# Optimization experiments

Hardware: AMD Instinct MI355X
Metric: run time of the kernel (lower is better)

## Reference

```python
import jax, jax.numpy as jnp
import numpy as np

ROUTING_ITERATIONS = 3
EPS = 1e-8


def squash(s):
    # standard CapsNet squash along the last (channels_per_unit) axis
    sq = jnp.sum(s * s, axis=-1, keepdims=True)
    return (sq / (1.0 + sq)) * s / jnp.sqrt(sq + EPS)


def setup_inputs() -> dict:
    key = jax.random.key(0)
    k1, k2 = jax.random.split(key)
    # inputs: (batch, input_channels, input_units)
    inputs = jax.random.normal(k1, (32, 8, 1152), dtype=jnp.float32)
    # weights: (input_units, num_units, input_channels, channels_per_unit)
    weights = jax.random.normal(k2, (1152, 10, 8, 16), dtype=jnp.float32)
    return {"inputs": inputs, "weights": weights}


def reference(inputs, weights):
    # (B, C, U) -> (B, U, C)
    votes = jnp.transpose(inputs, (0, 2, 1))
    # broadcast to (B, U, N, C, D): elementwise product as in the torch code
    pondered = weights[None, :, :, :, :] * votes[:, :, None, :, None]
    logits = jnp.zeros_like(pondered)
    out = pondered  # placeholder; overwritten in first iteration
    for _ in range(ROUTING_ITERATIONS):
        couplings = jax.nn.softmax(logits, axis=-1)
        out = squash(couplings * pondered)
        logits = logits + pondered * out  # agreement update
    # (B, U, N, C, D) -> (B, N, U, C, D)
    return jnp.transpose(out, (0, 2, 1, 3, 4))
```

## Files before the change

kernel.cpp:

```cpp
#include <hip/hip_runtime.h>

#define BB 32
#define UU 1152
#define NN 10
#define CC 8
#define DD 16
#define EPS 1e-8f
#define INV_LN2 1.44269504088896341f


typedef float f32x4 __attribute__((ext_vector_type(4)));

__device__ __forceinline__ float rcp_fast(float x) { return __builtin_amdgcn_rcpf(x); }
__device__ __forceinline__ float rsq_fast(float x) { return __builtin_amdgcn_rsqf(x); }

#if __has_builtin(__builtin_amdgcn_exp2f)
__device__ __forceinline__ float exp2_fast(float x) { return __builtin_amdgcn_exp2f(x); }
#else
__device__ __forceinline__ float exp2_fast(float x) { return __expf(x * 0.6931471805599453f); }
#endif

__device__ __forceinline__ float pair_sum(float x) {
    float y = __int_as_float(
        __builtin_amdgcn_update_dpp(0, __float_as_int(x), 0xB1, 0xF, 0xF, true));
    return x + y;
}

__device__ __forceinline__ float hsum4(f32x4 a) {
    return (a.x + a.y) + (a.z + a.w);
}

__device__ __forceinline__ f32x4 exp2_v4(f32x4 a) {
    f32x4 r;
    r.x = exp2_fast(a.x); r.y = exp2_fast(a.y);
    r.z = exp2_fast(a.z); r.w = exp2_fast(a.w);
    return r;
}

__global__ __launch_bounds__(256) void caps_route_kernel(
    const float* __restrict__ inputs,
    const float* __restrict__ weights,
    float* __restrict__ out)
{
    int tid = threadIdx.x;
    int bi  = blockIdx.x;
    int b   = bi & 31;
    int ub  = bi >> 5;

    int sub    = tid & 1;
    int c      = (tid >> 1) & 7;
    int ulocal = tid >> 4;
    int u      = ub * 16 + ulocal;

    float v = inputs[(b * CC + c) * UU + u];

    const float* wbase = weights + (u * NN * CC + c) * DD + sub * 8;
    float*       obase = out + ((b * NN * UU + u) * CC + c) * DD + sub * 8;
    const int WSTRIDE = CC * DD;
    const int OSTRIDE = UU * CC * DD;

    f32x4 wa0 = *reinterpret_cast<const f32x4*>(wbase);
    f32x4 wb0 = *reinterpret_cast<const f32x4*>(wbase + 4);
    f32x4 wa1 = *reinterpret_cast<const f32x4*>(wbase + WSTRIDE);
    f32x4 wb1 = *reinterpret_cast<const f32x4*>(wbase + WSTRIDE + 4);

    #pragma unroll 1
    for (int n = 0; n < NN; ++n) {
        f32x4 wa = wa0, wb = wb0;
        wa0 = wa1; wb0 = wb1;
        int np = (n + 2 < NN) ? (n + 2) : (NN - 1);
        wa1 = *reinterpret_cast<const f32x4*>(wbase + np * WSTRIDE);
        wb1 = *reinterpret_cast<const f32x4*>(wbase + np * WSTRIDE + 4);

        f32x4 pa = wa * v, pb = wb * v;
        f32x4 qa = pa * pa, qb = pb * pb;

        float sq0 = pair_sum(hsum4(qa + qb)) * (1.0f / 256.0f);
        float kk = sq0 * rcp_fast(1.0f + sq0) * rsq_fast(sq0 + EPS)
                   * (INV_LN2 / 16.0f);
        f32x4 La = kk * qa, Lb = kk * qb;

        {
            f32x4 ea = exp2_v4(La), eb = exp2_v4(Lb);
            float S = pair_sum(hsum4(ea + eb));
            f32x4 ma = ea * qa, mb = eb * qb;
            float A = pair_sum(hsum4(ma * ea + mb * eb));
            float Ssq = S * S;
            float k = A * rsq_fast(fmaf(EPS, Ssq, A)) * rcp_fast(Ssq + A)
                      * INV_LN2;
            La += k * ma;  Lb += k * mb;
        }

        {
            f32x4 ea = exp2_v4(La), eb = exp2_v4(Lb);
            float S = pair_sum(hsum4(ea + eb));
            f32x4 ta = ea * pa, tb = eb * pb;
            float A = pair_sum(hsum4(ta * ta + tb * tb));
            float Ssq = S * S;
            float ko = A * rsq_fast(fmaf(EPS, Ssq, A)) * rcp_fast(Ssq + A);
            *reinterpret_cast<f32x4*>(obase + n * OSTRIDE)     = ko * ta;
            *reinterpret_cast<f32x4*>(obase + n * OSTRIDE + 4) = ko * tb;
        }
    }
}

extern "C" void kernel_launch(void* const* d_in, const int* in_sizes, int n_in,
                              void* d_out, int out_size, void* d_ws, size_t ws_size,
                              hipStream_t stream) {
    const float* inputs  = (const float*)d_in[0];
    const float* weights = (const float*)d_in[1];
    float* out = (float*)d_out;

    const long long total = (long long)BB * UU * CC * 2;
    const int block = 256;
    const int grid = (int)(total / block);
    caps_route_kernel<<<grid, block, 0, stream>>>(inputs, weights, out);
}
```

Before: 43.52 us.

## Precompute per-slice weight squared norms in a side kernel to skip first reduction

Adds a pre-pass kernel that computes the sum of squares of each 16-element weight row into the workspace. The routing kernel then gets the first squared norm as v^2 times that table entry instead of doing a cross-lane reduction. The change also drops the two-deep software prefetch of weights in favour of plain per-iteration loads, and raises occupancy via launch_bounds(256,8). The extra kernel launch and workspace traffic may cost more than the few saved instructions; whether the table path runs depends on the workspace size.

```diff
diff --git a/kernel.cpp b/kernel.cpp
--- a/kernel.cpp
+++ b/kernel.cpp
@@ -37,9 +37,24 @@
     return r;
 }
 
-__global__ __launch_bounds__(256) void caps_route_kernel(
+__global__ __launch_bounds__(256) void w2_kernel(
+    const float* __restrict__ weights, float* __restrict__ w2)
+{
+    int idx = blockIdx.x * blockDim.x + threadIdx.x;
+    const float* wp = weights + (long long)idx * DD;
+    f32x4 a = *reinterpret_cast<const f32x4*>(wp);
+    f32x4 b = *reinterpret_cast<const f32x4*>(wp + 4);
+    f32x4 c = *reinterpret_cast<const f32x4*>(wp + 8);
+    f32x4 d = *reinterpret_cast<const f32x4*>(wp + 12);
+    f32x4 s = a * a + b * b + c * c + d * d;
+    w2[idx] = hsum4(s);
+}
+
+template <bool USE_W2>
+__global__ __launch_bounds__(256, 8) void caps_route_kernel(
     const float* __restrict__ inputs,
     const float* __restrict__ weights,
+    const float* __restrict__ w2tab,
     float* __restrict__ out)
 {
     int tid = threadIdx.x;
@@ -52,30 +67,30 @@
     int ulocal = tid >> 4;
     int u      = ub * 16 + ulocal;
 
-    float v = inputs[(b * CC + c) * UU + u];
+    float v  = inputs[(b * CC + c) * UU + u];
+    float v2 = v * v * (1.0f / 256.0f);
 
-    const float* wbase = weights + (u * NN * CC + c) * DD + sub * 8;
+    int wslice = (u * NN + 0) * CC + c;
+    const float* wbase = weights + wslice * DD + sub * 8;
+    const float* w2p   = w2tab + wslice;
     float*       obase = out + ((b * NN * UU + u) * CC + c) * DD + sub * 8;
     const int WSTRIDE = CC * DD;
     const int OSTRIDE = UU * CC * DD;
 
-    f32x4 wa0 = *reinterpret_cast<const f32x4*>(wbase);
-    f32x4 wb0 = *reinterpret_cast<const f32x4*>(wbase + 4);
-    f32x4 wa1 = *reinterpret_cast<const f32x4*>(wbase + WSTRIDE);
-    f32x4 wb1 = *reinterpret_cast<const f32x4*>(wbase + WSTRIDE + 4);
-
     #pragma unroll 1
     for (int n = 0; n < NN; ++n) {
-        f32x4 wa = wa0, wb = wb0;
-        wa0 = wa1; wb0 = wb1;
-        int np = (n + 2 < NN) ? (n + 2) : (NN - 1);
-        wa1 = *reinterpret_cast<const f32x4*>(wbase + np * WSTRIDE);
-        wb1 = *reinterpret_cast<const f32x4*>(wbase + np * WSTRIDE + 4);
+        f32x4 wa = *reinterpret_cast<const f32x4*>(wbase + n * WSTRIDE);
+        f32x4 wb = *reinterpret_cast<const f32x4*>(wbase + n * WSTRIDE + 4);
 
         f32x4 pa = wa * v, pb = wb * v;
         f32x4 qa = pa * pa, qb = pb * pb;
 
-        float sq0 = pair_sum(hsum4(qa + qb)) * (1.0f / 256.0f);
+        float sq0;
+        if (USE_W2) {
+            sq0 = v2 * w2p[n * CC];
+        } else {
+            sq0 = pair_sum(hsum4(qa + qb)) * (1.0f / 256.0f);
+        }
         float kk = sq0 * rcp_fast(1.0f + sq0) * rsq_fast(sq0 + EPS)
                    * (INV_LN2 / 16.0f);
         f32x4 La = kk * qa, Lb = kk * qb;
@@ -111,8 +126,18 @@
     const float* weights = (const float*)d_in[1];
     float* out = (float*)d_out;
 
+    const int W2N = UU * NN * CC;
+    const bool use_w2 = (ws_size >= (size_t)W2N * sizeof(float));
+
     const long long total = (long long)BB * UU * CC * 2;
     const int block = 256;
     const int grid = (int)(total / block);
-    caps_route_kernel<<<grid, block, 0, stream>>>(inputs, weights, out);
+
+    if (use_w2) {
+        float* w2 = (float*)d_ws;
+        w2_kernel<<<W2N / 256, 256, 0, stream>>>(weights, w2);
+        caps_route_kernel<true><<<grid, block, 0, stream>>>(inputs, weights, w2, out);
+    } else {
+        caps_route_kernel<false><<<grid, block, 0, stream>>>(inputs, weights, nullptr, out);
+    }
 }
```

Result: slower. 48.10 us (+10.5%).
